# Performance work log

Hardware: AMD Instinct MI355X
Metric: run time of the kernel (lower is better)

The kernel has to match this reference:

```python
import jax, jax.numpy as jnp
import numpy as np

B, S, F, H, NL, T = 64, 512, 256, 512, 1, 96
HA = H // 8  # attention hidden size (scale_factor=8)


def _p(key, shape, scale=0.05):
    return jax.random.normal(key, shape, dtype=jnp.float32) * scale


def setup_inputs() -> dict:
    key = jax.random.key(0)
    ks = jax.random.split(key, 20)
    return {
        "input_seq": jax.random.normal(ks[0], (B, S, F), dtype=jnp.float32),
        "h0": jax.random.normal(ks[1], (B, H), dtype=jnp.float32),
        "c0": jax.random.normal(ks[2], (B, H), dtype=jnp.float32),
        # encoder LSTM (torch gate order i,f,g,o), combined bias b_ih+b_hh
        "W_ih_e": _p(ks[3], (4 * H, F)),
        "W_hh_e": _p(ks[4], (4 * H, H)),
        "b_e": _p(ks[5], (4 * H,)),
        # decoder LSTM
        "W_ih_d": _p(ks[6], (4 * H, F)),
        "W_hh_d": _p(ks[7], (4 * H, H)),
        "b_d": _p(ks[8], (4 * H,)),
        # attention
        "We_p": _p(ks[9], (HA, H)),
        "be_p": _p(ks[10], (HA,)),
        "Wh_p": _p(ks[11], (HA, H)),
        "bh_p": _p(ks[12], (HA,)),
        "Wa": _p(ks[13], (HA, 2 * HA)),
        "ba": _p(ks[14], (HA,)),
        "v": jax.random.uniform(ks[15], (HA,), dtype=jnp.float32),
        # output linear: (H + HA) -> F
        "Wo": _p(ks[16], (F, H + HA)),
        "bo": _p(ks[17], (F,)),
        "output_size": T,
    }


def _lstm_step(x, h, c, Wih, Whh, b):
    gates = x @ Wih.T + h @ Whh.T + b  # (B, 4H)
    i, f, g, o = jnp.split(gates, 4, axis=-1)
    i, f, o = jax.nn.sigmoid(i), jax.nn.sigmoid(f), jax.nn.sigmoid(o)
    c = f * c + i * jnp.tanh(g)
    h = o * jnp.tanh(c)
    return h, c


def reference(input_seq, h0, c0, W_ih_e, W_hh_e, b_e, W_ih_d, W_hh_d, b_d,
              We_p, be_p, Wh_p, bh_p, Wa, ba, v, Wo, bo, output_size):
    # ---- encoder LSTM over seq (time-major scan) ----
    xs = jnp.swapaxes(input_seq, 0, 1)  # (S, B, F)

    def enc_step(carry, x):
        h, c = carry
        h, c = _lstm_step(x, h, c, W_ih_e, W_hh_e, b_e)
        return (h, c), h

    (h, c), enc_hs = jax.lax.scan(enc_step, (h0, c0), xs)
    enc_out = jnp.swapaxes(enc_hs, 0, 1)  # (B, S, H)

    # encoder projection (same every decode step; hoisted)
    enc_proj = enc_out @ We_p.T + be_p  # (B, S, HA)
    # split attn Linear weight: first HA cols act on hidden, last HA on enc_proj
    Wa_h, Wa_e = Wa[:, :HA], Wa[:, HA:]
    enc_attn = enc_proj @ Wa_e.T  # (B, S, HA)

    def dec_step(carry, _):
        x, h, c = carry
        # Bahdanau attention (uses pre-LSTM hidden h, per original)
        hq = h @ Wh_p.T + bh_p  # (B, HA)
        energy = jnp.tanh(hq[:, None, :] @ Wa_h.T + enc_attn + ba)  # (B, S, HA)
        scores = jnp.einsum('bsh,h->bs', energy, v)
        aw = jax.nn.softmax(scores, axis=1)  # (B, S)
        ctx = jnp.einsum('bs,bsh->bh', aw, enc_proj)  # (B, HA)
        # single-step decoder LSTM
        h, c = _lstm_step(x, h, c, W_ih_d, W_hh_d, b_d)
        out = jnp.concatenate([h, ctx], axis=1) @ Wo.T + bo  # (B, F)
        return (out, h, c), out

    carry0 = (input_seq[:, -1, :], h, c)
    _, preds = jax.lax.scan(dec_step, carry0, None, length=output_size)  # (T, B, F)
    # outputs[:, :, t] = pred_t; return outputs[:, -1, :] -> last feature over time
    return preds[:, :, -1].T  # (B, T)
```

## Files before the change

kernel.cpp:

```cpp
#include <hip/hip_runtime.h>


namespace {

typedef float nfloat4 __attribute__((ext_vector_type(4)));

__device__ __forceinline__ float4 nt_load4(const float4* p) {
    nfloat4 r = __builtin_nontemporal_load((const nfloat4*)p);
    return make_float4(r.x, r.y, r.z, r.w);
}

__device__ __forceinline__ float fsigmoid(float x) {
    return 1.0f / (1.0f + __expf(-x));
}
__device__ __forceinline__ float ftanh(float x) {
    float e = __expf(2.0f * x);
    return 1.0f - 2.0f / (e + 1.0f);
}

__device__ __forceinline__ void coh_store(float* p, float v) {
    __hip_atomic_store(p, v, __ATOMIC_RELAXED, __HIP_MEMORY_SCOPE_AGENT);
}
__device__ __forceinline__ void coh_store2(float* p, float2 v) {
    union { float2 f; unsigned long long u; } cv; cv.f = v;
    __hip_atomic_store((unsigned long long*)p, cv.u,
                       __ATOMIC_RELAXED, __HIP_MEMORY_SCOPE_AGENT);
}

__device__ __forceinline__ void post_flag(unsigned* flag, unsigned val) {
    if (threadIdx.x == 0) {
        asm volatile("s_waitcnt vmcnt(0)" ::: "memory");
        __hip_atomic_store(flag, val, __ATOMIC_RELAXED, __HIP_MEMORY_SCOPE_AGENT);
    }
}
__device__ __forceinline__ void wait_group(const unsigned* flags, int base,
                                           int mask, unsigned val) {
    const unsigned* f = flags + base + (threadIdx.x & mask);
    for (;;) {
        unsigned x = __hip_atomic_load(f, __ATOMIC_RELAXED, __HIP_MEMORY_SCOPE_AGENT);
        if (__all(x >= val)) break;
        __builtin_amdgcn_s_sleep(1);
    }
    asm volatile("" ::: "memory");
}
__device__ __forceinline__ void wait_lstm_inputs(const unsigned* attnF,
                                                 const unsigned* lstmF,
                                                 int w, unsigned val) {
    int lane = threadIdx.x & 63;
    const unsigned* fa = attnF + lane * 2;
    const unsigned* fl = lstmF + (w & 3) * 32 + (lane & 31);
    for (;;) {
        unsigned a = __hip_atomic_load(fa + 0, __ATOMIC_RELAXED, __HIP_MEMORY_SCOPE_AGENT);
        unsigned b = __hip_atomic_load(fa + 1, __ATOMIC_RELAXED, __HIP_MEMORY_SCOPE_AGENT);
        unsigned c = __hip_atomic_load(fl,     __ATOMIC_RELAXED, __HIP_MEMORY_SCOPE_AGENT);
        int ok = (a >= val) && (b >= val) && (c >= val);
        if (__all(ok)) break;
        __builtin_amdgcn_s_sleep(1);
    }
    asm volatile("" ::: "memory");
}

__global__ __launch_bounds__(256) void k_transpose_input(
    const float* __restrict__ in, float4* __restrict__ xQ)
{
    __shared__ float tile[64][65];
    int s  = blockIdx.x >> 2;
    int f0 = (blockIdx.x & 3) * 64;
    int lane = threadIdx.x & 63;
    int r0   = threadIdx.x >> 6;
    for (int r = r0; r < 64; r += 4)
        tile[r][lane] = in[(size_t)r * (512 * 256) + s * 256 + f0 + lane];
    __syncthreads();
    for (int q = r0; q < 16; q += 4) {
        float4 vv = make_float4(tile[lane][4*q], tile[lane][4*q+1],
                                tile[lane][4*q+2], tile[lane][4*q+3]);
        xQ[((size_t)s * 64 + (f0 >> 2) + q) * 64 + lane] = vv;
    }
}

__global__ __launch_bounds__(256) void k_prep(
    const float* __restrict__ We_p, const float* __restrict__ Wh_p,
    const float* __restrict__ h0,   const float* __restrict__ c0,
    const float* __restrict__ Wa,
    float* __restrict__ We_pT, float* __restrict__ Wh_pT,
    float* __restrict__ encH0, float* __restrict__ cT,
    float* __restrict__ WahT,  float* __restrict__ WaeT)
{
    int idx = blockIdx.x * blockDim.x + threadIdx.x;
    const int total = 32768 * 4 + 4096 * 2;
    for (; idx < total; idx += gridDim.x * blockDim.x) {
        if (idx < 32768) {
            int u = idx >> 6, h = idx & 63;
            We_pT[idx] = We_p[h * 512 + u];
        } else if (idx < 65536) {
            int i2 = idx - 32768; int k = i2 >> 6, i = i2 & 63;
            Wh_pT[i2] = Wh_p[i * 512 + k];
        } else if (idx < 98304) {
            int i2 = idx - 65536; int u = i2 >> 6, b = i2 & 63;
            encH0[(u >> 2) * 256 + b * 4 + (u & 3)] = h0[b * 512 + u];
        } else if (idx < 131072) {
            int i2 = idx - 98304; int u = i2 >> 6, b = i2 & 63;
            cT[i2] = c0[b * 512 + u];
        } else if (idx < 135168) {
            int i2 = idx - 131072; int j = i2 >> 6, i = i2 & 63;
            WahT[i2] = Wa[i * 128 + j];
        } else {
            int i2 = idx - 135168; int h2 = i2 >> 6, h = i2 & 63;
            WaeT[i2] = Wa[h * 128 + 64 + h2];
        }
    }
}

__global__ __launch_bounds__(256) void k_prep_wcomb(
    const float* __restrict__ Wih, const float* __restrict__ Whh,
    const float* __restrict__ Wo,  const float* __restrict__ bd,
    const float* __restrict__ bo,
    float* __restrict__ Wh, float* __restrict__ Wc, float* __restrict__ bprime)
{
    int r = blockIdx.x;
    for (int j = threadIdx.x; j < 576; j += 256) {
        float acc = 0.f;
        for (int f = 0; f < 256; ++f)
            acc = fmaf(Wih[r * 256 + f], Wo[f * 576 + j], acc);
        if (j < 512) Wh[(size_t)r * 512 + j] = acc + Whh[(size_t)r * 512 + j];
        else         Wc[(size_t)r * 64 + (j - 512)] = acc;
    }
    if (threadIdx.x == 0) {
        float s = bd[r];
        for (int f = 0; f < 256; ++f)
            s = fmaf(Wih[r * 256 + f], bo[f], s);
        bprime[r] = s;
    }
}

__global__ __launch_bounds__(256) void k_prep_g0(
    const float4* __restrict__ xQlast, const float* __restrict__ Wih,
    const float* __restrict__ bd, float* __restrict__ g0)
{
    int r = blockIdx.x * 4 + ((int)threadIdx.x >> 6);
    int lane = threadIdx.x & 63;
    const float4* Wih4 = (const float4*)Wih;
    float acc = bd[r];
    for (int q = 0; q < 64; ++q) {
        float4 a  = xQlast[q * 64 + lane];
        float4 wv = Wih4[(size_t)r * 64 + q];
        acc = fmaf(a.x, wv.x, acc); acc = fmaf(a.y, wv.y, acc);
        acc = fmaf(a.z, wv.z, acc); acc = fmaf(a.w, wv.w, acc);
    }
    g0[(size_t)r * 64 + lane] = acc;
}

template<int NQ>
__device__ __forceinline__ void accum_seg_pf(
    float acc[8], const float4* __restrict__ actQ, int qb,
    const float4* __restrict__ W4, int wstride, int u0, int lane)
{
    float4 a[NQ];
    #pragma unroll
    for (int q = 0; q < NQ; ++q)
        a[q] = nt_load4(&actQ[(qb + q) * 64 + lane]);
    #pragma unroll
    for (int q = 0; q < NQ; ++q) {
        #pragma unroll
        for (int uu = 0; uu < 2; ++uu)
            #pragma unroll
            for (int g = 0; g < 4; ++g) {
                float4 wv = W4[(size_t)(g * 512 + u0 + uu) * wstride + (qb + q)];
                float& A = acc[uu * 4 + g];
                A = fmaf(a[q].x, wv.x, A); A = fmaf(a[q].y, wv.y, A);
                A = fmaf(a[q].z, wv.z, A); A = fmaf(a[q].w, wv.w, A);
            }
    }
}

__device__ __forceinline__ void accum_ctx_reg(
    float acc[8], float4 c0, float4 c1,
    const float4* __restrict__ Wc4, int u0, int w)
{
    #pragma unroll
    for (int uu = 0; uu < 2; ++uu)
        #pragma unroll
        for (int g = 0; g < 4; ++g) {
            float4 w0 = Wc4[(size_t)(g * 512 + u0 + uu) * 16 + w * 2 + 0];
            float4 w1 = Wc4[(size_t)(g * 512 + u0 + uu) * 16 + w * 2 + 1];
            float& A = acc[uu * 4 + g];
            A = fmaf(c0.x, w0.x, A); A = fmaf(c0.y, w0.y, A);
            A = fmaf(c0.z, w0.z, A); A = fmaf(c0.w, w0.w, A);
            A = fmaf(c1.x, w1.x, A); A = fmaf(c1.y, w1.y, A);
            A = fmaf(c1.z, w1.z, A); A = fmaf(c1.w, w1.w, A);
        }
}

__device__ __forceinline__ void lstm_finish_vec(
    int u0, int tid, int w, float acc[8], float2& creg,
    const float* __restrict__ addVec, float* __restrict__ houtSlot, float* smem)
{
    int lane = tid & 63;
    float* part = smem;
    float* gsum = smem + 4096;
    #pragma unroll
    for (int r = 0; r < 8; ++r)
        part[(w * 8 + r) * 64 + lane] = acc[r];
    __syncthreads();
    {
        int b = tid & 63, r = tid >> 6;
        float s = 0.f;
        #pragma unroll
        for (int ww = 0; ww < 8; ++ww)
            s += part[(ww * 8 + r) * 64 + b];
        gsum[r * 64 + b] = s;
    }
    __syncthreads();
    if (tid < 64) {
        int b = tid;
        float cc[2] = {creg.x, creg.y};
        float hv[2];
        #pragma unroll
        for (int uu = 0; uu < 2; ++uu) {
            int u = u0 + uu;
            float gi = gsum[(uu*4+0)*64 + b] + addVec[u];
            float gf = gsum[(uu*4+1)*64 + b] + addVec[512 + u];
            float gg = gsum[(uu*4+2)*64 + b] + addVec[1024 + u];
            float go = gsum[(uu*4+3)*64 + b] + addVec[1536 + u];
            float si = fsigmoid(gi), sf = fsigmoid(gf), so = fsigmoid(go);
            float tg = ftanh(gg);
            float cn = sf * cc[uu] + si * tg;
            cc[uu] = cn;
            hv[uu] = so * ftanh(cn);
        }
        creg = make_float2(cc[0], cc[1]);
        coh_store2(houtSlot + (u0 >> 2) * 256 + b * 4 + (u0 & 3),
                   make_float2(hv[0], hv[1]));
    }
}

__device__ __forceinline__ void lstm_finish_row(
    int u0, int tid, int w, float acc[8], float2& creg,
    const float* __restrict__ addRowB, float* __restrict__ houtSlot, float* smem)
{
    int lane = tid & 63;
    float* part = smem;
    float* gsum = smem + 4096;
    #pragma unroll
    for (int r = 0; r < 8; ++r)
        part[(w * 8 + r) * 64 + lane] = acc[r];
    __syncthreads();
    {
        int b = tid & 63, r = tid >> 6;
        float s = 0.f;
        #pragma unroll
        for (int ww = 0; ww < 8; ++ww)
            s += part[(ww * 8 + r) * 64 + b];
        gsum[r * 64 + b] = s;
    }
    __syncthreads();
    if (tid < 64) {
        int b = tid;
        float cc[2] = {creg.x, creg.y};
        float hv[2];
        #pragma unroll
        for (int uu = 0; uu < 2; ++uu) {
            int u = u0 + uu;
            float gi = gsum[(uu*4+0)*64 + b] + addRowB[(size_t)(0 * 512 + u) * 64 + b];
            float gf = gsum[(uu*4+1)*64 + b] + addRowB[(size_t)(1 * 512 + u) * 64 + b];
            float gg = gsum[(uu*4+2)*64 + b] + addRowB[(size_t)(2 * 512 + u) * 64 + b];
            float go = gsum[(uu*4+3)*64 + b] + addRowB[(size_t)(3 * 512 + u) * 64 + b];
            float si = fsigmoid(gi), sf = fsigmoid(gf), so = fsigmoid(go);
            float tg = ftanh(gg);
            float cn = sf * cc[uu] + si * tg;
            cc[uu] = cn;
            hv[uu] = so * ftanh(cn);
        }
        creg = make_float2(cc[0], cc[1]);
        coh_store2(houtSlot + (u0 >> 2) * 256 + b * 4 + (u0 & 3),
                   make_float2(hv[0], hv[1]));
    }
}

__global__ __launch_bounds__(512, 2) void k_enc_persistent(
    const float4* __restrict__ xQ, float* __restrict__ encH,
    float* __restrict__ cT,
    const float* __restrict__ Wih, const float* __restrict__ Whh,
    const float* __restrict__ bias, unsigned* flags)
{
    __shared__ float smem[4608];
    int tid = threadIdx.x;
    int lane = tid & 63;
    int w = __builtin_amdgcn_readfirstlane(tid >> 6);
    int bi = blockIdx.x;
    int u0 = bi * 2;
    const float4* Wih4 = (const float4*)Wih;
    const float4* Whh4 = (const float4*)Whh;
    float2 creg = make_float2(0.f, 0.f);
    if (tid < 64) { creg.x = cT[u0 * 64 + tid]; creg.y = cT[(u0 + 1) * 64 + tid]; }
    float acc[8];
    #pragma unroll
    for (int r = 0; r < 8; ++r) acc[r] = 0.f;
    accum_seg_pf<8>(acc, xQ, w * 8, Wih4, 64, u0, lane);
    for (int t = 0; t < 512; ++t) {
        wait_group(flags, w * 32, 31, (unsigned)t);
        accum_seg_pf<16>(acc, (const float4*)(encH + (size_t)t * 32768),
                         w * 16, Whh4, 128, u0, lane);
        lstm_finish_vec(u0, tid, w, acc, creg, bias,
                        encH + (size_t)(t + 1) * 32768, smem);
        post_flag(&flags[bi], (unsigned)(t + 1));
        #pragma unroll
        for (int r = 0; r < 8; ++r) acc[r] = 0.f;
        if (t + 1 < 512)
            accum_seg_pf<8>(acc, xQ + (size_t)(t + 1) * 4096, w * 8, Wih4, 64, u0, lane);
    }
    if (tid < 64) { cT[u0 * 64 + tid] = creg.x; cT[(u0 + 1) * 64 + tid] = creg.y; }
}

__global__ __launch_bounds__(256) void k_proj_attn(
    const float* __restrict__ encH,  const float* __restrict__ We_pT,
    const float* __restrict__ be_p,  const float* __restrict__ WaeT,
    const float* __restrict__ ba,
    float* __restrict__ encProj, float* __restrict__ attnPre)
{
    int lane = threadIdx.x & 63;
    int w    = __builtin_amdgcn_readfirstlane((int)threadIdx.x >> 6);
    int wid  = blockIdx.x * 4 + w;
    int b    = wid >> 6;
    int soct = wid & 63;
    float acc[8];
    float bep = be_p[lane];
    #pragma unroll
    for (int j = 0; j < 8; ++j) acc[j] = bep;
    #pragma unroll 2
    for (int q = 0; q < 128; ++q) {
        float w0 = We_pT[(4*q+0) * 64 + lane];
        float w1 = We_pT[(4*q+1) * 64 + lane];
        float w2 = We_pT[(4*q+2) * 64 + lane];
        float w3 = We_pT[(4*q+3) * 64 + lane];
        #pragma unroll
        for (int j = 0; j < 8; ++j) {
            const float4* hb4 = (const float4*)(encH + (size_t)(soct*8 + j + 1) * 32768);
            float4 hv = hb4[q * 64 + b];
            acc[j] = fmaf(hv.x, w0, acc[j]); acc[j] = fmaf(hv.y, w1, acc[j]);
            acc[j] = fmaf(hv.z, w2, acc[j]); acc[j] = fmaf(hv.w, w3, acc[j]);
        }
    }
    #pragma unroll
    for (int j = 0; j < 8; ++j)
        encProj[((size_t)b * 512 + soct * 8 + j) * 64 + lane] = acc[j];
    #pragma unroll
    for (int j = 0; j < 8; ++j) {
        float aa = ba[lane];
        for (int h2 = 0; h2 < 64; ++h2)
            aa = fmaf(__shfl(acc[j], h2), WaeT[h2 * 64 + lane], aa);
        attnPre[((size_t)b * 512 + soct * 8 + j) * 64 + lane] = aa;
    }
}

__global__ __launch_bounds__(256) void k_attn_transpose(
    const float* __restrict__ attnPre, float* __restrict__ attnPreT)
{
    __shared__ float tile[64][65];
    int b  = blockIdx.x >> 3;
    int s0 = (blockIdx.x & 7) * 64;
    int lane = threadIdx.x & 63;
    int r0   = threadIdx.x >> 6;
    for (int r = r0; r < 64; r += 4)
        tile[r][lane] = attnPre[(size_t)b * 32768 + (size_t)(s0 + r) * 64 + lane];
    __syncthreads();
    for (int r = r0; r < 64; r += 4)
        attnPreT[(size_t)b * 32768 + (size_t)r * 512 + s0 + lane] = tile[lane][r];
}

__device__ __forceinline__ void attention_half(
    int b, int tid, int w, int lane,
    const float* __restrict__ hcur,
    const float* __restrict__ Wh_pT, const float* __restrict__ bh_p,
    const float* __restrict__ WahT,  const float* __restrict__ v,
    const float* __restrict__ apL,
    const float* __restrict__ epL,
    float* __restrict__ ctxsumOut,
    float* __restrict__ mSOut,
    float* smem)
{
    float* hq  = smem;
    float* hWa = smem + 64;
    float* sc  = smem + 128;
    float* part = smem + 384;
    float* red  = smem + 896;
    {
        const float4* h4 = (const float4*)hcur;
        float4 hv[16];
        #pragma unroll
        for (int j = 0; j < 16; ++j)
            hv[j] = h4[(w * 16 + j) * 64 + b];
        float p = 0.f;
        #pragma unroll
        for (int j = 0; j < 16; ++j) {
            int q = w * 16 + j;
            p = fmaf(hv[j].x, Wh_pT[(4*q+0) * 64 + lane], p);
            p = fmaf(hv[j].y, Wh_pT[(4*q+1) * 64 + lane], p);
            p = fmaf(hv[j].z, Wh_pT[(4*q+2) * 64 + lane], p);
            p = fmaf(hv[j].w, Wh_pT[(4*q+3) * 64 + lane], p);
        }
        part[w * 64 + lane] = p;
    }
    __syncthreads();
    if (tid < 64) {
        float s = bh_p[tid];
        #pragma unroll
        for (int ww = 0; ww < 8; ++ww) s += part[ww * 64 + tid];
        hq[tid] = s;
    }
    __syncthreads();
    if (tid < 64) {
        float s = 0.f;
        for (int j = 0; j < 64; ++j)
            s = fmaf(hq[j], WahT[j * 64 + tid], s);
        hWa[tid] = s;
    }
    __syncthreads();
    {
        int sp  = tid & 255;
        int hh0 = (tid >> 8) * 32;
        float acc = 0.f;
        for (int j = 0; j < 32; ++j) {
            int h = hh0 + j;
            float e = ftanh(hWa[h] + apL[h * 256 + sp]);
            acc = fmaf(v[h], e, acc);
        }
        part[tid] = acc;
    }
    __syncthreads();
    if (tid < 256)
        sc[tid] = part[tid] + part[256 + tid];
    __syncthreads();
    if (tid < 256) {
        float x = sc[tid];
        float m = x;
        #pragma unroll
        for (int off = 32; off > 0; off >>= 1)
            m = fmaxf(m, __shfl_xor(m, off));
        if (lane == 0) red[w] = m;
    }
    __syncthreads();
    if (tid == 0)
        red[8] = fmaxf(fmaxf(red[0], red[1]), fmaxf(red[2], red[3]));
    __syncthreads();
    float M = red[8];
    if (tid < 256) {
        float e = __expf(sc[tid] - M);
        sc[tid] = e;
        float s = e;
        #pragma unroll
        for (int off = 32; off > 0; off >>= 1)
            s += __shfl_xor(s, off);
        if (lane == 0) red[w] = s;
    }
    __syncthreads();
    if (tid == 0)
        red[9] = ((red[0] + red[1]) + (red[2] + red[3]));
    __syncthreads();
    {
        float a = 0.f;
        for (int i = 0; i < 32; ++i) {
            int sp2 = w * 32 + i;
            a = fmaf(sc[sp2], epL[sp2 * 64 + lane], a);
        }
        part[w * 64 + lane] = a;
    }
    __syncthreads();
    if (tid < 64) {
        float s = 0.f;
        #pragma unroll
        for (int ww = 0; ww < 8; ++ww) s += part[ww * 64 + tid];
        coh_store(&ctxsumOut[(tid >> 2) * 256 + b * 4 + (tid & 3)], s);
    }
    if (tid == 0) {
        coh_store(&mSOut[b], M);
        coh_store(&mSOut[64 + b], red[9]);
    }
    __syncthreads();
}

__device__ __forceinline__ void load_ctx_quads(
    int t, int w, int lane,
    const float* __restrict__ ctxsumH, const float* __restrict__ mSbuf,
    float4& c0, float4& c1)
{
    const float* mS = mSbuf + (size_t)(t - 1) * 256;
    float m0 = mS[lane],       S0 = mS[64 + lane];
    float m1 = mS[128 + lane], S1 = mS[192 + lane];
    float M  = fmaxf(m0, m1);
    float e0 = __expf(m0 - M), e1 = __expf(m1 - M);
    float inv = 1.0f / (e0 * S0 + e1 * S1);
    e0 *= inv; e1 *= inv;
    const float4* a0 = (const float4*)(ctxsumH + (size_t)(t - 1) * 8192);
    const float4* a1 = (const float4*)(ctxsumH + (size_t)(t - 1) * 8192 + 4096);
    float4 x0 = a0[(w * 2 + 0) * 64 + lane];
    float4 y0 = a1[(w * 2 + 0) * 64 + lane];
    float4 x1 = a0[(w * 2 + 1) * 64 + lane];
    float4 y1 = a1[(w * 2 + 1) * 64 + lane];
    c0 = make_float4(e0 * x0.x + e1 * y0.x, e0 * x0.y + e1 * y0.y,
                     e0 * x0.z + e1 * y0.z, e0 * x0.w + e1 * y0.w);
    c1 = make_float4(e0 * x1.x + e1 * y1.x, e0 * x1.y + e1 * y1.y,
                     e0 * x1.z + e1 * y1.z, e0 * x1.w + e1 * y1.w);
}

extern __shared__ float dynsmem[];
__global__ __launch_bounds__(512) void k_dec_persistent(
    const float* __restrict__ encHend,
    float* __restrict__ dechH,
    float* __restrict__ cT,
    const float* __restrict__ Whh,
    const float* __restrict__ Wh,
    const float* __restrict__ Wc,
    const float* __restrict__ g0, const float* __restrict__ bprime,
    const float* __restrict__ Wh_pT, const float* __restrict__ bh_p,
    const float* __restrict__ WahT,  const float* __restrict__ v,
    const float* __restrict__ attnPreT, const float* __restrict__ encProj,
    float* __restrict__ ctxsumH,
    float* __restrict__ mSbuf,
    unsigned* attnFlags, unsigned* lstmFlags)
{
    float* smem = dynsmem;
    float* apL  = dynsmem + 4608;
    float* epL  = apL + 16384;
    int tid = threadIdx.x;
    int lane = tid & 63;
    int w = __builtin_amdgcn_readfirstlane(tid >> 6);
    int bi = blockIdx.x;
    if (bi < 128) {
        int b = bi & 63, half = bi >> 6;
        {
            const float4* src = (const float4*)(attnPreT + (size_t)b * 32768 + half * 256);
            float4* dst = (float4*)apL;
            for (int i = tid; i < 4096; i += 512) {
                int h = i >> 6, qc = i & 63;
                dst[i] = src[(size_t)h * 128 + qc];
            }
        }
        {
            const float4* src = (const float4*)(encProj + ((size_t)b * 512 + half * 256) * 64);
            float4* dst = (float4*)epL;
            for (int i = tid; i < 4096; i += 512)
                dst[i] = src[i];
        }
        __syncthreads();
        for (int t = 0; t < 96; ++t) {
            if (t) wait_group(lstmFlags, (w & 3) * 32, 31, (unsigned)t);
            const float* hc = t ? dechH + (size_t)(t - 1) * 32768 : encHend;
            attention_half(b, tid, w, lane, hc, Wh_pT, bh_p, WahT, v,
                           apL, epL,
                           ctxsumH + (size_t)t * 8192 + half * 4096,
                           mSbuf + (size_t)t * 256 + half * 128, smem);
            post_flag(&attnFlags[bi], (unsigned)(t + 1));
        }
    } else {
        int u0A = (bi - 128) * 2;
        int u0B = u0A + 256;
        const float4* Whh4 = (const float4*)Whh;
        const float4* Wh4  = (const float4*)Wh;
        const float4* Wc4  = (const float4*)Wc;
        float2 cA = make_float2(0.f, 0.f), cB = cA;
        if (tid < 64) {
            cA.x = cT[u0A * 64 + tid]; cA.y = cT[(u0A + 1) * 64 + tid];
            cB.x = cT[u0B * 64 + tid]; cB.y = cT[(u0B + 1) * 64 + tid];
        }
        for (int t = 0; t < 96; ++t) {
            if (t) wait_lstm_inputs(attnFlags, lstmFlags, w, (unsigned)t);
            const float* hc = t ? dechH + (size_t)(t - 1) * 32768 : encHend;
            float* hn = dechH + (size_t)t * 32768;
            float acc[8];
            if (t == 0) {
                #pragma unroll
                for (int r = 0; r < 8; ++r) acc[r] = 0.f;
                accum_seg_pf<16>(acc, (const float4*)hc, w * 16, Whh4, 128, u0A, lane);
                lstm_finish_row(u0A, tid, w, acc, cA, g0, hn, smem);
                #pragma unroll
                for (int r = 0; r < 8; ++r) acc[r] = 0.f;
                accum_seg_pf<16>(acc, (const float4*)hc, w * 16, Whh4, 128, u0B, lane);
                lstm_finish_row(u0B, tid, w, acc, cB, g0, hn, smem);
            } else {
                float4 cq0, cq1;
                load_ctx_quads(t, w, lane, ctxsumH, mSbuf, cq0, cq1);
                #pragma unroll
                for (int r = 0; r < 8; ++r) acc[r] = 0.f;
                accum_seg_pf<16>(acc, (const float4*)hc, w * 16, Wh4, 128, u0A, lane);
                accum_ctx_reg(acc, cq0, cq1, Wc4, u0A, w);
                lstm_finish_vec(u0A, tid, w, acc, cA, bprime, hn, smem);
                #pragma unroll
                for (int r = 0; r < 8; ++r) acc[r] = 0.f;
                accum_seg_pf<16>(acc, (const float4*)hc, w * 16, Wh4, 128, u0B, lane);
                accum_ctx_reg(acc, cq0, cq1, Wc4, u0B, w);
                lstm_finish_vec(u0B, tid, w, acc, cB, bprime, hn, smem);
            }
            post_flag(&lstmFlags[bi - 128], (unsigned)(t + 1));
        }
    }
}

__global__ __launch_bounds__(256) void k_dout(
    const float* __restrict__ dechH,
    const float* __restrict__ ctxsumH, const float* __restrict__ mSbuf,
    const float* __restrict__ Wo, const float* __restrict__ bo,
    float* __restrict__ dout)
{
    __shared__ float part[256];
    int tau = blockIdx.x;
    int tid = threadIdx.x;
    int lane = tid & 63;
    int w = tid >> 6;
    const float* hq = dechH + (size_t)tau * 32768;
    const float* wrow = Wo + 255 * 576;
    float acc = 0.f;
    for (int i = w * 128; i < w * 128 + 128; ++i)
        acc = fmaf(wrow[i], hq[(i >> 2) * 256 + lane * 4 + (i & 3)], acc);
    part[w * 64 + lane] = acc;
    __syncthreads();
    if (tid < 64) {
        int b = tid;
        const float* mS = mSbuf + (size_t)tau * 256;
        float m0 = mS[b],       S0 = mS[64 + b];
        float m1 = mS[128 + b], S1 = mS[192 + b];
        float M  = fmaxf(m0, m1);
        float e0 = __expf(m0 - M), e1 = __expf(m1 - M);
        float inv = 1.0f / (e0 * S0 + e1 * S1);
        e0 *= inv; e1 *= inv;
        const float* cs0 = ctxsumH + (size_t)tau * 8192;
        const float* cs1 = cs0 + 4096;
        float a2 = bo[255];
        for (int h2 = 0; h2 < 64; ++h2) {
            int idx = (h2 >> 2) * 256 + b * 4 + (h2 & 3);
            a2 = fmaf(wrow[512 + h2], e0 * cs0[idx] + e1 * cs1[idx], a2);
        }
        float s = a2 + part[b] + part[64 + b] + part[128 + b] + part[192 + b];
        dout[b * 96 + tau] = s;
    }
}

}

extern "C" void kernel_launch(void* const* d_in, const int* in_sizes, int n_in,
                              void* d_out, int out_size, void* d_ws, size_t ws_size,
                              hipStream_t stream)
{
    (void)in_sizes; (void)n_in; (void)out_size; (void)ws_size;
    const float* input_seq = (const float*)d_in[0];
    const float* h0     = (const float*)d_in[1];
    const float* c0     = (const float*)d_in[2];
    const float* W_ih_e = (const float*)d_in[3];
    const float* W_hh_e = (const float*)d_in[4];
    const float* b_e    = (const float*)d_in[5];
    const float* W_ih_d = (const float*)d_in[6];
    const float* W_hh_d = (const float*)d_in[7];
    const float* b_d    = (const float*)d_in[8];
    const float* We_p   = (const float*)d_in[9];
    const float* be_p   = (const float*)d_in[10];
    const float* Wh_p   = (const float*)d_in[11];
    const float* bh_p   = (const float*)d_in[12];
    const float* Wa     = (const float*)d_in[13];
    const float* ba     = (const float*)d_in[14];
    const float* v      = (const float*)d_in[15];
    const float* Wo     = (const float*)d_in[16];
    const float* bo     = (const float*)d_in[17];
    float* out = (float*)d_out;

    unsigned* encFlags  = (unsigned*)d_ws;
    unsigned* attnFlags = encFlags + 256;
    unsigned* lstmFlags = attnFlags + 128;
    float* ws       = (float*)d_ws + 1024;
    float* xT       = ws;
    float* encH     = xT + 8388608;
    float* cT       = encH + 16809984;
    float* We_pT    = cT + 32768;
    float* Wh_pT    = We_pT + 32768;
    float* WahT     = Wh_pT + 32768;
    float* WaeT     = WahT + 4096;
    float* encProj  = WaeT + 4096;
    float* attnPre  = encProj + 2097152;
    float* dechH    = attnPre + 2097152;
    float* ctxsumH  = dechH + 3145728;
    float* mSbuf    = ctxsumH + 786432;
    float* Wh       = mSbuf + 24576;
    float* Wc       = Wh + 1048576;
    float* bprime   = Wc + 131072;
    float* g0       = bprime + 2048;
    float* attnPreT = xT;

    (void)hipFuncSetAttribute((const void*)k_dec_persistent,
                              hipFuncAttributeMaxDynamicSharedMemorySize, 149504);

    (void)hipMemsetAsync(d_ws, 0, 4096, stream);
    k_transpose_input<<<2048, 256, 0, stream>>>(input_seq, (float4*)xT);
    k_prep<<<544, 256, 0, stream>>>(We_p, Wh_p, h0, c0, Wa,
                                    We_pT, Wh_pT, encH, cT, WahT, WaeT);
    k_prep_wcomb<<<2048, 256, 0, stream>>>(W_ih_d, W_hh_d, Wo, b_d, bo,
                                           Wh, Wc, bprime);
    k_prep_g0<<<512, 256, 0, stream>>>((const float4*)(xT + (size_t)511 * 16384),
                                       W_ih_d, b_d, g0);
    k_enc_persistent<<<256, 512, 0, stream>>>((const float4*)xT, encH, cT,
                                              W_ih_e, W_hh_e, b_e, encFlags);
    k_proj_attn<<<1024, 256, 0, stream>>>(encH, We_pT, be_p, WaeT, ba,
                                          encProj, attnPre);
    k_attn_transpose<<<512, 256, 0, stream>>>(attnPre, attnPreT);
    k_dec_persistent<<<256, 512, 149504, stream>>>(encH + (size_t)512 * 32768,
                                                   dechH, cT,
                                                   W_hh_d, Wh, Wc, g0, bprime,
                                                   Wh_pT, bh_p, WahT, v,
                                                   attnPreT, encProj,
                                                   ctxsumH, mSbuf,
                                                   attnFlags, lstmFlags);
    k_dout<<<96, 256, 0, stream>>>(dechH, ctxsumH, mSbuf, Wo, bo, out);
}
```

Before: 6.206 ms.

## Merge two LSTM row-pair passes per decoder step into one fused reduction

The decoder LSTM blocks now accumulate both of their row pairs in a single pass over the hidden activations. They then reduce both partial sets through one shared-memory exchange, with 128 threads finishing the gates in parallel. This removes one activation load pass and several __syncthreads per step. The cross-warp sum is folded into the gate threads, and the nontemporal loads are dropped. The cost is more registers (two accumulator sets), a larger shared-memory layout, and an explicit vmcnt wait before the trailing barrier.

```diff
diff --git a/kernel.cpp b/kernel.cpp
--- a/kernel.cpp
+++ b/kernel.cpp
@@ -2,13 +2,6 @@
 
 
 namespace {
-
-typedef float nfloat4 __attribute__((ext_vector_type(4)));
-
-__device__ __forceinline__ float4 nt_load4(const float4* p) {
-    nfloat4 r = __builtin_nontemporal_load((const nfloat4*)p);
-    return make_float4(r.x, r.y, r.z, r.w);
-}
 
 __device__ __forceinline__ float fsigmoid(float x) {
     return 1.0f / (1.0f + __expf(-x));
@@ -158,7 +151,7 @@
     float4 a[NQ];
     #pragma unroll
     for (int q = 0; q < NQ; ++q)
-        a[q] = nt_load4(&actQ[(qb + q) * 64 + lane]);
+        a[q] = actQ[(qb + q) * 64 + lane];
     #pragma unroll
     for (int q = 0; q < NQ; ++q) {
         #pragma unroll
@@ -169,6 +162,33 @@
                 float& A = acc[uu * 4 + g];
                 A = fmaf(a[q].x, wv.x, A); A = fmaf(a[q].y, wv.y, A);
                 A = fmaf(a[q].z, wv.z, A); A = fmaf(a[q].w, wv.w, A);
+            }
+    }
+}
+
+template<int NQ>
+__device__ __forceinline__ void accum_seg_pf2(
+    float accA[8], float accB[8], const float4* __restrict__ actQ, int qb,
+    const float4* __restrict__ W4, int wstride, int u0A, int u0B, int lane)
+{
+    float4 a[NQ];
+    #pragma unroll
+    for (int q = 0; q < NQ; ++q)
+        a[q] = actQ[(qb + q) * 64 + lane];
+    #pragma unroll
+    for (int q = 0; q < NQ; ++q) {
+        #pragma unroll
+        for (int uu = 0; uu < 2; ++uu)
+            #pragma unroll
+            for (int g = 0; g < 4; ++g) {
+                float4 wA = W4[(size_t)(g * 512 + u0A + uu) * wstride + (qb + q)];
+                float4 wB = W4[(size_t)(g * 512 + u0B + uu) * wstride + (qb + q)];
+                float& A = accA[uu * 4 + g];
+                float& Bv = accB[uu * 4 + g];
+                A = fmaf(a[q].x, wA.x, A); A = fmaf(a[q].y, wA.y, A);
+                A = fmaf(a[q].z, wA.z, A); A = fmaf(a[q].w, wA.w, A);
+                Bv = fmaf(a[q].x, wB.x, Bv); Bv = fmaf(a[q].y, wB.y, Bv);
+                Bv = fmaf(a[q].z, wB.z, Bv); Bv = fmaf(a[q].w, wB.w, Bv);
             }
     }
 }
@@ -234,39 +254,46 @@
     }
 }
 
-__device__ __forceinline__ void lstm_finish_row(
-    int u0, int tid, int w, float acc[8], float2& creg,
-    const float* __restrict__ addRowB, float* __restrict__ houtSlot, float* smem)
+template<bool ROWADD>
+__device__ __forceinline__ void lstm_finish2(
+    int u0A, int u0B, int tid, int w, float accA[8], float accB[8],
+    float2& creg, const float* __restrict__ addVec,
+    const float* __restrict__ addRowB,
+    float* __restrict__ houtSlot, float* smem)
 {
     int lane = tid & 63;
     float* part = smem;
-    float* gsum = smem + 4096;
     #pragma unroll
     for (int r = 0; r < 8; ++r)
-        part[(w * 8 + r) * 64 + lane] = acc[r];
-    __syncthreads();
-    {
-        int b = tid & 63, r = tid >> 6;
-        float s = 0.f;
-        #pragma unroll
-        for (int ww = 0; ww < 8; ++ww)
-            s += part[(ww * 8 + r) * 64 + b];
-        gsum[r * 64 + b] = s;
-    }
-    __syncthreads();
-    if (tid < 64) {
-        int b = tid;
+        part[(w * 16 + r) * 64 + lane] = accA[r];
+    #pragma unroll
+    for (int r = 0; r < 8; ++r)
+        part[(w * 16 + 8 + r) * 64 + lane] = accB[r];
+    __syncthreads();
+    if (tid < 128) {
+        int b  = tid & 63;
+        int ps = tid >> 6;
+        int u0 = ps ? u0B : u0A;
         float cc[2] = {creg.x, creg.y};
         float hv[2];
         #pragma unroll
         for (int uu = 0; uu < 2; ++uu) {
             int u = u0 + uu;
-            float gi = gsum[(uu*4+0)*64 + b] + addRowB[(size_t)(0 * 512 + u) * 64 + b];
-            float gf = gsum[(uu*4+1)*64 + b] + addRowB[(size_t)(1 * 512 + u) * 64 + b];
-            float gg = gsum[(uu*4+2)*64 + b] + addRowB[(size_t)(2 * 512 + u) * 64 + b];
-            float go = gsum[(uu*4+3)*64 + b] + addRowB[(size_t)(3 * 512 + u) * 64 + b];
-            float si = fsigmoid(gi), sf = fsigmoid(gf), so = fsigmoid(go);
-            float tg = ftanh(gg);
+            float gate[4];
+            #pragma unroll
+            for (int g = 0; g < 4; ++g) {
+                int row = ps * 8 + uu * 4 + g;
+                float s = 0.f;
+                #pragma unroll
+                for (int ww = 0; ww < 8; ++ww)
+                    s += part[(ww * 16 + row) * 64 + b];
+                if (ROWADD) s += addRowB[(size_t)(g * 512 + u) * 64 + b];
+                else        s += addVec[g * 512 + u];
+                gate[g] = s;
+            }
+            float si = fsigmoid(gate[0]), sf = fsigmoid(gate[1]);
+            float so = fsigmoid(gate[3]);
+            float tg = ftanh(gate[2]);
             float cn = sf * cc[uu] + si * tg;
             cc[uu] = cn;
             hv[uu] = so * ftanh(cn);
@@ -274,7 +301,9 @@
         creg = make_float2(cc[0], cc[1]);
         coh_store2(houtSlot + (u0 >> 2) * 256 + b * 4 + (u0 & 3),
                    make_float2(hv[0], hv[1]));
-    }
+        asm volatile("s_waitcnt vmcnt(0)" ::: "memory");
+    }
+    __syncthreads();
 }
 
 __global__ __launch_bounds__(512, 2) void k_enc_persistent(
@@ -520,7 +549,7 @@
     unsigned* attnFlags, unsigned* lstmFlags)
 {
     float* smem = dynsmem;
-    float* apL  = dynsmem + 4608;
+    float* apL  = dynsmem + 8192;
     float* epL  = apL + 16384;
     int tid = threadIdx.x;
     int lane = tid & 63;
@@ -558,38 +587,34 @@
         const float4* Whh4 = (const float4*)Whh;
         const float4* Wh4  = (const float4*)Wh;
         const float4* Wc4  = (const float4*)Wc;
-        float2 cA = make_float2(0.f, 0.f), cB = cA;
+        float2 creg = make_float2(0.f, 0.f);
         if (tid < 64) {
-            cA.x = cT[u0A * 64 + tid]; cA.y = cT[(u0A + 1) * 64 + tid];
-            cB.x = cT[u0B * 64 + tid]; cB.y = cT[(u0B + 1) * 64 + tid];
+            creg.x = cT[u0A * 64 + tid]; creg.y = cT[(u0A + 1) * 64 + tid];
+        } else if (tid < 128) {
+            creg.x = cT[u0B * 64 + (tid - 64)];
+            creg.y = cT[(u0B + 1) * 64 + (tid - 64)];
         }
         for (int t = 0; t < 96; ++t) {
             if (t) wait_lstm_inputs(attnFlags, lstmFlags, w, (unsigned)t);
             const float* hc = t ? dechH + (size_t)(t - 1) * 32768 : encHend;
             float* hn = dechH + (size_t)t * 32768;
-            float acc[8];
+            float accA[8], accB[8];
+            #pragma unroll
+            for (int r = 0; r < 8; ++r) { accA[r] = 0.f; accB[r] = 0.f; }
             if (t == 0) {
-                #pragma unroll
-                for (int r = 0; r < 8; ++r) acc[r] = 0.f;
-                accum_seg_pf<16>(acc, (const float4*)hc, w * 16, Whh4, 128, u0A, lane);
-                lstm_finish_row(u0A, tid, w, acc, cA, g0, hn, smem);
-                #pragma unroll
-                for (int r = 0; r < 8; ++r) acc[r] = 0.f;
-                accum_seg_pf<16>(acc, (const float4*)hc, w * 16, Whh4, 128, u0B, lane);
-                lstm_finish_row(u0B, tid, w, acc, cB, g0, hn, smem);
+                accum_seg_pf2<16>(accA, accB, (const float4*)hc, w * 16,
+                                  Whh4, 128, u0A, u0B, lane);
+                lstm_finish2<true>(u0A, u0B, tid, w, accA, accB, creg,
+                                   nullptr, g0, hn, smem);
             } else {
                 float4 cq0, cq1;
                 load_ctx_quads(t, w, lane, ctxsumH, mSbuf, cq0, cq1);
-                #pragma unroll
-                for (int r = 0; r < 8; ++r) acc[r] = 0.f;
-                accum_seg_pf<16>(acc, (const float4*)hc, w * 16, Wh4, 128, u0A, lane);
-                accum_ctx_reg(acc, cq0, cq1, Wc4, u0A, w);
-                lstm_finish_vec(u0A, tid, w, acc, cA, bprime, hn, smem);
-                #pragma unroll
-                for (int r = 0; r < 8; ++r) acc[r] = 0.f;
-                accum_seg_pf<16>(acc, (const float4*)hc, w * 16, Wh4, 128, u0B, lane);
-                accum_ctx_reg(acc, cq0, cq1, Wc4, u0B, w);
-                lstm_finish_vec(u0B, tid, w, acc, cB, bprime, hn, smem);
+                accum_seg_pf2<16>(accA, accB, (const float4*)hc, w * 16,
+                                  Wh4, 128, u0A, u0B, lane);
+                accum_ctx_reg(accA, cq0, cq1, Wc4, u0A, w);
+                accum_ctx_reg(accB, cq0, cq1, Wc4, u0B, w);
+                lstm_finish2<false>(u0A, u0B, tid, w, accA, accB, creg,
+                                    bprime, nullptr, hn, smem);
             }
             post_flag(&lstmFlags[bi - 128], (unsigned)(t + 1));
         }
@@ -685,7 +710,7 @@
     float* attnPreT = xT;
 
     (void)hipFuncSetAttribute((const void*)k_dec_persistent,
-                              hipFuncAttributeMaxDynamicSharedMemorySize, 149504);
+                              hipFuncAttributeMaxDynamicSharedMemorySize, 163840);
 
     (void)hipMemsetAsync(d_ws, 0, 4096, stream);
     k_transpose_input<<<2048, 256, 0, stream>>>(input_seq, (float4*)xT);
@@ -700,7 +725,7 @@
     k_proj_attn<<<1024, 256, 0, stream>>>(encH, We_pT, be_p, WaeT, ba,
                                           encProj, attnPre);
     k_attn_transpose<<<512, 256, 0, stream>>>(attnPre, attnPreT);
-    k_dec_persistent<<<256, 512, 149504, stream>>>(encH + (size_t)512 * 32768,
+    k_dec_persistent<<<256, 512, 152576, stream>>>(encH + (size_t)512 * 32768,
                                                    dechH, cT,
                                                    W_hh_d, Wh, Wc, g0, bprime,
                                                    Wh_pT, bh_p, WahT, v,
```

After: 5.554 ms. 10.5% less time.
